# Kernel optimization log

Measured on AMD Instinct MI355X. Metric: run time of the kernel, lower is better.

The kernel has to match this reference:

```python
import jax, jax.numpy as jnp
import numpy as np

N_NODES = 100000
N_EDGES = 1600000
HID = 150
N_LAYERS = 5


def setup_inputs() -> dict:
    key = jax.random.key(0)
    ks = jax.random.split(key, 7)
    s = 1.0 / np.sqrt(HID)
    return {
        "x": jax.random.normal(ks[0], (N_NODES, HID), dtype=jnp.float32),
        "weight": jax.random.uniform(ks[1], (N_LAYERS, HID, HID), jnp.float32, -s, s),
        "w_ih": jax.random.uniform(ks[2], (3 * HID, HID), jnp.float32, -s, s),
        "w_hh": jax.random.uniform(ks[3], (3 * HID, HID), jnp.float32, -s, s),
        "b_ih": jax.random.uniform(ks[4], (3 * HID,), jnp.float32, -s, s),
        "b_hh": jax.random.uniform(ks[5], (3 * HID,), jnp.float32, -s, s),
        "edge_index": jax.random.randint(ks[6], (2, N_EDGES), 0, N_NODES, dtype=jnp.int32),
    }


def _gru_cell(inp, h, w_ih, w_hh, b_ih, b_hh):
    # torch.nn.GRUCell math
    gi = inp @ w_ih.T + b_ih            # [N, 3H]
    gh = h @ w_hh.T + b_hh              # [N, 3H]
    i_r, i_z, i_n = jnp.split(gi, 3, axis=-1)
    h_r, h_z, h_n = jnp.split(gh, 3, axis=-1)
    r = jax.nn.sigmoid(i_r + h_r)
    z = jax.nn.sigmoid(i_z + h_z)
    n = jnp.tanh(i_n + r * h_n)
    return (1.0 - z) * n + z * h


def reference(x, weight, w_ih, w_hh, b_ih, b_hh, edge_index):
    # GatedGraphConv: h'_i = GRU( sum_{j->i} (h_j @ W_l), h_i ), repeated num_layers times
    src, dst = edge_index[0], edge_index[1]
    n_nodes = x.shape[0]
    h = x
    for l in range(weight.shape[0]):
        m = h @ weight[l]                                        # [N, H] transform
        aggr = jax.ops.segment_sum(m[src], dst, num_segments=n_nodes)  # scatter-add over edges
        h = _gru_cell(aggr, h, w_ih, w_hh, b_ih, b_hh)
    return h
```

## Files before the change

kernel.cpp:

```cpp
#include <hip/hip_runtime.h>
#include <hip/hip_bf16.h>
#include <cmath>

#define HID 150
#define NN 100000
#define NE 1600000
#define NL 5
#define G3 (3*HID)
#define KP 320
#define NP 640
#define KS 10
#define BM 64
#define HSTEPS 20
#define HS_BF (20*64*8)

#define NPBSH 9
#define NBK 196
#define CAPL 64
#define CAPG 10240
#define CHUNK 4096
#define BPAD 16

typedef __hip_bfloat16 bf16;
using short8 = __attribute__((ext_vector_type(8))) short;
using f32x4  = __attribute__((ext_vector_type(4))) float;

static __device__ __forceinline__ unsigned short bf_bits(float v) {
    __hip_bfloat16 h = __float2bfloat16(v);
    return *reinterpret_cast<unsigned short*>(&h);
}

static __device__ __forceinline__ float blo(unsigned int p) {
    return __uint_as_float((p & 0xffffu) << 16);
}
static __device__ __forceinline__ float bhi(unsigned int p) {
    return __uint_as_float(p & 0xffff0000u);
}

static __device__ __forceinline__ void gld_lds16(const void* g, void* l) {
    __builtin_amdgcn_global_load_lds(
        (const __attribute__((address_space(1))) void*)g,
        (__attribute__((address_space(3))) void*)l, 16, 0, 0);
}

__global__ void build_wfrag(const float* __restrict__ W, const float* __restrict__ w_ih,
                            const float* __restrict__ w_hh, const float* __restrict__ b_ih,
                            const float* __restrict__ b_hh, bf16* __restrict__ wfrag) {
    int idx = blockIdx.x * 256 + threadIdx.x;
    if (idx >= NL * KP * NP) return;
    int j = idx % NP;
    int k = (idx / NP) % KP;
    int l = idx / (NP * KP);
    int sec = j / 160;
    int f = j - sec * 160;
    float v = 0.f;
    if (f < HID) {
        if (k < HID) {
            if (sec < 3) {
                const float* Wl = W + (size_t)l * HID * HID + (size_t)k * HID;
                const float* wr = w_ih + (size_t)(sec * HID + f) * HID;
                float acc = 0.f;
                for (int t = 0; t < HID; ++t) acc += Wl[t] * wr[t];
                v = acc;
            }
        } else if (k == HID) {
            v = (sec == 0) ? b_ih[f] + b_hh[f]
              : (sec == 1) ? b_ih[HID + f] + b_hh[HID + f]
              : (sec == 2) ? b_ih[2 * HID + f]
                           : b_hh[2 * HID + f];
        } else if (k >= 160 && k < 160 + HID) {
            int kk = k - 160;
            if (sec == 0)      v = w_hh[(size_t)f * HID + kk];
            else if (sec == 1) v = w_hh[(size_t)(HID + f) * HID + kk];
            else if (sec == 3) v = w_hh[(size_t)(2 * HID + f) * HID + kk];
        }
    }
    int kstep = k >> 5, kq = (k >> 3) & 3, ki = k & 7;
    int half = sec >> 1, s2 = sec & 1;
    int fgroup = f >> 4, nl = j & 15;
    int tl = s2 * 10 + fgroup;
    int lane = kq * 16 + nl;
    size_t addr = ((((size_t)(l * KS + kstep) * 2 + half) * 20 + tl) * 64 + lane) * 8 + ki;
    wfrag[addr] = __float2bfloat16(v);
}

__global__ __launch_bounds__(256)
void bin_edges(const int* __restrict__ ei, int* __restrict__ bcnt,
               unsigned int* __restrict__ bbuf) {
    __shared__ int lcnt[NBK];
    __shared__ unsigned int lstage[NBK * CAPL];
    int t = threadIdx.x;
    for (int i = t; i < NBK; i += 256) lcnt[i] = 0;
    __syncthreads();
    int e0 = blockIdx.x * CHUNK;
#pragma unroll
    for (int it = 0; it < CHUNK / 256; ++it) {
        int e = e0 + it * 256 + t;
        if (e < NE) {
            int src = ei[e], dst = ei[NE + e];
            int b = dst >> NPBSH;
            unsigned int v = (unsigned int)src | ((unsigned int)(dst & 511) << 17);
            int li = atomicAdd(&lcnt[b], 1);
            if (li < CAPL) {
                lstage[b * CAPL + li] = v;
            } else {
                int gp = atomicAdd(&bcnt[b * BPAD], 1);
                if (gp < CAPG) bbuf[(size_t)b * CAPG + gp] = v;
            }
        }
    }
    __syncthreads();
    int wave = t >> 6, lane = t & 63;
    for (int b = wave; b < NBK; b += 4) {
        int cnt = lcnt[b];
        if (cnt > CAPL) cnt = CAPL;
        if (cnt == 0) continue;
        int base = 0;
        if (lane == 0) base = atomicAdd(&bcnt[b * BPAD], cnt);
        base = __shfl(base, 0, 64);
        if (lane < cnt && base + lane < CAPG)
            bbuf[(size_t)b * CAPG + base + lane] = lstage[b * CAPL + lane];
    }
}

__global__ __launch_bounds__(256)
void csr_from_buckets(const int* __restrict__ bcnt, const unsigned int* __restrict__ bbuf,
                      int* __restrict__ off, int* __restrict__ csr) {
    __shared__ int hist[512];
    __shared__ int s[256];
    int b = blockIdx.x, t = threadIdx.x;
    hist[t] = 0;
    hist[256 + t] = 0;
    int base = 0;
    for (int i = 0; i < b; ++i) {
        int c = bcnt[i * BPAD];
        base += (c > CAPG) ? CAPG : c;
    }
    int cnt = bcnt[b * BPAD];
    if (cnt > CAPG) cnt = CAPG;
    __syncthreads();
    for (int i = t; i < cnt; i += 256) {
        unsigned int v = bbuf[(size_t)b * CAPG + i];
        atomicAdd(&hist[v >> 17], 1);
    }
    __syncthreads();
    int a0 = hist[2 * t], a1 = hist[2 * t + 1];
    int tsum = a0 + a1;
    s[t] = tsum;
    __syncthreads();
    for (int d = 1; d < 256; d <<= 1) {
        int u = (t >= d) ? s[t - d] : 0;
        __syncthreads();
        s[t] += u;
        __syncthreads();
    }
    int tb = base + s[t] - tsum;
    hist[2 * t] = tb;
    hist[2 * t + 1] = tb + a0;
    int node = (b << NPBSH) + 2 * t;
    if (node < NN) off[node] = tb;
    if (node + 1 < NN) off[node + 1] = tb + a0;
    if (b == NBK - 1 && t == 255) off[NN] = base + s[255];
    __syncthreads();
    for (int i = t; i < cnt; i += 256) {
        unsigned int v = bbuf[(size_t)b * CAPG + i];
        int p = atomicAdd(&hist[v >> 17], 1);
        csr[p] = (int)(v & 0x1FFFFu);
    }
}

__global__ void init_h(const float* __restrict__ x, bf16* __restrict__ Abuf) {
    size_t i = (size_t)blockIdx.x * 256 + threadIdx.x;
    if (i >= (size_t)NN * HID) return;
    int m = (int)(i / HID), f = (int)(i - (size_t)m * HID);
    Abuf[(size_t)m * KP + 160 + f] = __float2bfloat16(x[i]);
}

__global__ void aggregate(bf16* __restrict__ Abuf, const int* __restrict__ off,
                          const int* __restrict__ csr) {
    int node = (blockIdx.x * blockDim.x + threadIdx.x) >> 6;
    int lane = threadIdx.x & 63;
    if (node >= NN) return;
    int e0 = off[node], e1 = off[node + 1];
    float a0 = 0.f, a1 = 0.f, b0 = 0.f, b1 = 0.f;
    bool tail = lane < 11;
    int e = e0;
    for (; e + 4 <= e1; e += 4) {
        const unsigned int* r0 = (const unsigned int*)(Abuf + (size_t)csr[e]     * KP + 160);
        const unsigned int* r1 = (const unsigned int*)(Abuf + (size_t)csr[e + 1] * KP + 160);
        const unsigned int* r2 = (const unsigned int*)(Abuf + (size_t)csr[e + 2] * KP + 160);
        const unsigned int* r3 = (const unsigned int*)(Abuf + (size_t)csr[e + 3] * KP + 160);
        unsigned int p0 = r0[lane], p1 = r1[lane], p2 = r2[lane], p3 = r3[lane];
        unsigned int q0 = 0, q1 = 0, q2 = 0, q3 = 0;
        if (tail) { q0 = r0[64 + lane]; q1 = r1[64 + lane]; q2 = r2[64 + lane]; q3 = r3[64 + lane]; }
        a0 += blo(p0) + blo(p1) + blo(p2) + blo(p3);
        a1 += bhi(p0) + bhi(p1) + bhi(p2) + bhi(p3);
        b0 += blo(q0) + blo(q1) + blo(q2) + blo(q3);
        b1 += bhi(q0) + bhi(q1) + bhi(q2) + bhi(q3);
    }
    for (; e < e1; ++e) {
        const unsigned int* r = (const unsigned int*)(Abuf + (size_t)csr[e] * KP + 160);
        unsigned int p = r[lane];
        unsigned int q = tail ? r[64 + lane] : 0;
        a0 += blo(p); a1 += bhi(p);
        b0 += blo(q); b1 += bhi(q);
    }
    unsigned int* out = (unsigned int*)(Abuf + (size_t)node * KP);
    out[lane] = (unsigned int)bf_bits(a0) | ((unsigned int)bf_bits(a1) << 16);
    if (tail) out[64 + lane] = (unsigned int)bf_bits(b0) | ((unsigned int)bf_bits(b1) << 16);
    if (lane < 5) out[75 + lane] = (lane == 0) ? 0x00003F80u : 0u;
}

__global__ __launch_bounds__(256, 2)
void gemm_gru(const bf16* __restrict__ Abuf, const bf16* __restrict__ wfrag_l,
              float* __restrict__ h_out, bf16* __restrict__ Abuf_w, int last) {
    __shared__ __align__(16) bf16 As[KS * BM * 32];
    __shared__ __align__(16) bf16 Bs[2][HS_BF];
    int tid = threadIdx.x;
    int wave = tid >> 6, lane = tid & 63;
    int mh = wave >> 1, nh = wave & 1;
    int row0 = blockIdx.x * BM;

    {
        const char* gbase = (const char*)(Abuf + (size_t)row0 * KP);
        char* lbase = (char*)As;
#pragma unroll
        for (int it = 0; it < 10; ++it) {
            int c = it * 256 + tid;
            int ks = c >> 8;
            int rem = c & 255;
            int r = rem >> 2, qq = rem & 3;
            gld_lds16(gbase + (size_t)r * (KP * 2) + ks * 64 + qq * 16,
                      lbase + (size_t)c * 16);
        }
        const char* gb = (const char*)wfrag_l;
        char* lb = (char*)Bs[0];
#pragma unroll
        for (int it = 0; it < 5; ++it) {
            int c = it * 256 + tid;
            gld_lds16(gb + (size_t)c * 16, lb + (size_t)c * 16);
        }
    }
    __syncthreads();

    f32x4 acc[2][20];
#pragma unroll
    for (int mt = 0; mt < 2; ++mt)
#pragma unroll
        for (int t = 0; t < 20; ++t) acc[mt][t] = (f32x4){0.f, 0.f, 0.f, 0.f};

    int col = lane & 15, q = lane >> 4;
    short8 a0, a1;
    for (int hs = 0; hs < HSTEPS; ++hs) {
        int cur = hs & 1;
        if (hs < HSTEPS - 1) {
            const char* gb = (const char*)(wfrag_l + (size_t)(hs + 1) * HS_BF);
            char* lb = (char*)Bs[1 - cur];
#pragma unroll
            for (int it = 0; it < 5; ++it) {
                int c = it * 256 + tid;
                gld_lds16(gb + (size_t)c * 16, lb + (size_t)c * 16);
            }
        }
        int ks = hs >> 1, half = hs & 1;
        if (half == 0) {
            a0 = *(const short8*)(As + ((size_t)(ks * BM + mh * 32 + col) * 32 + q * 8));
            a1 = *(const short8*)(As + ((size_t)(ks * BM + mh * 32 + 16 + col) * 32 + q * 8));
        }
#pragma unroll
        for (int g = 0; g < 5; ++g) {
#pragma unroll
            for (int s2 = 0; s2 < 2; ++s2) {
                int tl = s2 * 10 + nh * 5 + g;
                short8 b = *(const short8*)(Bs[cur] + ((size_t)(tl * 64 + lane) * 8));
                int t = g * 4 + half * 2 + s2;
                acc[0][t] = __builtin_amdgcn_mfma_f32_16x16x32_bf16(a0, b, acc[0][t], 0, 0, 0);
                acc[1][t] = __builtin_amdgcn_mfma_f32_16x16x32_bf16(a1, b, acc[1][t], 0, 0, 0);
            }
        }
        __syncthreads();
    }

    int qrow = q * 4;
    bf16* Cs = &Bs[0][0];
#pragma unroll
    for (int mt = 0; mt < 2; ++mt) {
#pragma unroll
        for (int g = 0; g < 5; ++g) {
            int f = (nh * 5 + g) * 16 + col;
            if (f < HID) {
                f32x4 ar = acc[mt][g * 4 + 0], az = acc[mt][g * 4 + 1];
                f32x4 an = acc[mt][g * 4 + 2], ah = acc[mt][g * 4 + 3];
                int kh = 160 + f, ksh = kh >> 5, koff = kh & 31;
#pragma unroll
                for (int v = 0; v < 4; ++v) {
                    int rl = mh * 32 + mt * 16 + qrow + v;
                    float hp = __bfloat162float(As[((size_t)(ksh * BM) + rl) * 32 + koff]);
                    float r = 1.f / (1.f + __expf(-ar[v]));
                    float z = 1.f / (1.f + __expf(-az[v]));
                    float n = tanhf(an[v] + r * ah[v]);
                    float ho = (1.f - z) * n + z * hp;
                    if (last) {
                        int m = row0 + rl;
                        if (m < NN) h_out[(size_t)m * HID + f] = ho;
                    } else {
                        Cs[rl * 160 + f] = __float2bfloat16(ho);
                    }
                }
            }
        }
    }
    if (!last) {
        __syncthreads();
        const unsigned int* src = (const unsigned int*)Cs;
        for (int i = tid; i < 64 * 75; i += 256) {
            int r = i / 75, dw = i - r * 75;
            ((unsigned int*)(Abuf_w + (size_t)(row0 + r) * KP + 160))[dw] =
                src[r * 80 + dw];
        }
    }
}

extern "C" void kernel_launch(void* const* d_in, const int* in_sizes, int n_in,
                              void* d_out, int out_size, void* d_ws, size_t ws_size,
                              hipStream_t stream) {
    const float* x      = (const float*)d_in[0];
    const float* weight = (const float*)d_in[1];
    const float* w_ih   = (const float*)d_in[2];
    const float* w_hh   = (const float*)d_in[3];
    const float* b_ih   = (const float*)d_in[4];
    const float* b_hh   = (const float*)d_in[5];
    const int*   ei     = (const int*)d_in[6];
    float* h = (float*)d_out;

    const int nblk = (NN + BM - 1) / BM;
    const size_t NNP = (size_t)nblk * BM;
    char* p = (char*)d_ws;
    auto alloc = [&](size_t bytes) { char* r = p; p += (bytes + 255) & ~255ull; return r; };
    int*  off   = (int*)alloc((size_t)(NN + 1) * 4);
    int*  csr   = (int*)alloc((size_t)NE * 4);
    int*  bcnt  = (int*)alloc((size_t)NBK * BPAD * 4);
    unsigned int* bbuf = (unsigned int*)alloc((size_t)NBK * CAPG * 4);
    bf16* wfrag = (bf16*)alloc((size_t)NL * KS * 2 * HS_BF * 2);
    bf16* Abuf  = (bf16*)alloc((NNP + BM) * (size_t)KP * 2);

    hipMemsetAsync(bcnt, 0, (size_t)NBK * BPAD * 4, stream);
    build_wfrag<<<(NL * KP * NP + 255) / 256, 256, 0, stream>>>(weight, w_ih, w_hh, b_ih, b_hh, wfrag);
    bin_edges<<<(NE + CHUNK - 1) / CHUNK, 256, 0, stream>>>(ei, bcnt, bbuf);
    csr_from_buckets<<<NBK, 256, 0, stream>>>(bcnt, bbuf, off, csr);
    init_h<<<(int)(((size_t)NN * HID + 255) / 256), 256, 0, stream>>>(x, Abuf);

    for (int l = 0; l < NL; ++l) {
        aggregate<<<(NN * 64 + 255) / 256, 256, 0, stream>>>(Abuf, off, csr);
        gemm_gru<<<nblk, 256, 0, stream>>>(Abuf, wfrag + (size_t)l * KS * 2 * HS_BF,
                                           h, Abuf, (l == NL - 1) ? 1 : 0);
    }
}
```

Measured before the change: 1.195 ms.

## Stream A tiles through triple-buffered LDS with vmcnt-based pipelining in gemm_gru

The GEMM+GRU kernel no longer preloads the whole 64x320 A tile into LDS up front. A and B slices now go through three-stage ring buffers, prefetched two steps ahead, and explicit s_waitcnt vmcnt plus s_barrier replace __syncthreads. This shrinks LDS use, which may help occupancy, and overlaps the A loads with MFMA work. The cost is that the GRU epilogue now rereads the previous hidden state from global memory instead of LDS, and the hand-tuned vmcnt counts are fragile.

Result: faster. 1.111 ms (-7.0%).

```diff
diff --git a/kernel.cpp b/kernel.cpp
--- a/kernel.cpp
+++ b/kernel.cpp
@@ -214,34 +214,31 @@
 __global__ __launch_bounds__(256, 2)
 void gemm_gru(const bf16* __restrict__ Abuf, const bf16* __restrict__ wfrag_l,
               float* __restrict__ h_out, bf16* __restrict__ Abuf_w, int last) {
-    __shared__ __align__(16) bf16 As[KS * BM * 32];
-    __shared__ __align__(16) bf16 Bs[2][HS_BF];
+    __shared__ __align__(16) bf16 Bs[3][HS_BF];
+    __shared__ __align__(16) bf16 As3[3][BM * 32];
     int tid = threadIdx.x;
     int wave = tid >> 6, lane = tid & 63;
     int mh = wave >> 1, nh = wave & 1;
     int row0 = blockIdx.x * BM;
 
-    {
-        const char* gbase = (const char*)(Abuf + (size_t)row0 * KP);
-        char* lbase = (char*)As;
-#pragma unroll
-        for (int it = 0; it < 10; ++it) {
-            int c = it * 256 + tid;
-            int ks = c >> 8;
-            int rem = c & 255;
-            int r = rem >> 2, qq = rem & 3;
-            gld_lds16(gbase + (size_t)r * (KP * 2) + ks * 64 + qq * 16,
-                      lbase + (size_t)c * 16);
-        }
-        const char* gb = (const char*)wfrag_l;
-        char* lb = (char*)Bs[0];
+    const char* gbase = (const char*)(Abuf + (size_t)row0 * KP);
+    int ar = tid >> 2, aq = tid & 3;
+
+    auto stageB = [&](int hs) {
+        const char* gb = (const char*)(wfrag_l + (size_t)hs * HS_BF);
+        char* lb = (char*)Bs[hs % 3];
 #pragma unroll
         for (int it = 0; it < 5; ++it) {
             int c = it * 256 + tid;
             gld_lds16(gb + (size_t)c * 16, lb + (size_t)c * 16);
         }
-    }
-    __syncthreads();
+    };
+    auto stageA = [&](int ks) {
+        gld_lds16(gbase + (size_t)ar * (KP * 2) + ks * 64 + aq * 16,
+                  (char*)As3[ks % 3] + (size_t)tid * 16);
+    };
+
+    stageB(0); stageA(0); stageB(1); stageA(1);
 
     f32x4 acc[2][20];
 #pragma unroll
@@ -251,21 +248,19 @@
 
     int col = lane & 15, q = lane >> 4;
     short8 a0, a1;
+#pragma unroll
     for (int hs = 0; hs < HSTEPS; ++hs) {
-        int cur = hs & 1;
-        if (hs < HSTEPS - 1) {
-            const char* gb = (const char*)(wfrag_l + (size_t)(hs + 1) * HS_BF);
-            char* lb = (char*)Bs[1 - cur];
-#pragma unroll
-            for (int it = 0; it < 5; ++it) {
-                int c = it * 256 + tid;
-                gld_lds16(gb + (size_t)c * 16, lb + (size_t)c * 16);
-            }
-        }
-        int ks = hs >> 1, half = hs & 1;
+        if (hs < 18)       asm volatile("s_waitcnt vmcnt(6)" ::: "memory");
+        else if (hs == 18) asm volatile("s_waitcnt vmcnt(5)" ::: "memory");
+        else               asm volatile("s_waitcnt vmcnt(0)" ::: "memory");
+        __builtin_amdgcn_s_barrier();
+        __builtin_amdgcn_sched_barrier(0);
+
+        int ks = hs >> 1, half = hs & 1, cur = hs % 3;
         if (half == 0) {
-            a0 = *(const short8*)(As + ((size_t)(ks * BM + mh * 32 + col) * 32 + q * 8));
-            a1 = *(const short8*)(As + ((size_t)(ks * BM + mh * 32 + 16 + col) * 32 + q * 8));
+            const bf16* Ak = As3[ks % 3];
+            a0 = *(const short8*)(Ak + ((mh * 32 + col) * 32 + q * 8));
+            a1 = *(const short8*)(Ak + ((mh * 32 + 16 + col) * 32 + q * 8));
         }
 #pragma unroll
         for (int g = 0; g < 5; ++g) {
@@ -278,7 +273,8 @@
                 acc[1][t] = __builtin_amdgcn_mfma_f32_16x16x32_bf16(a1, b, acc[1][t], 0, 0, 0);
             }
         }
-        __syncthreads();
+        if (hs + 2 < HSTEPS) stageB(hs + 2);
+        if (half == 1 && ks + 2 < KS) stageA(ks + 2);
     }
 
     int qrow = q * 4;
@@ -289,14 +285,13 @@
         for (int g = 0; g < 5; ++g) {
             int f = (nh * 5 + g) * 16 + col;
             if (f < HID) {
-                f32x4 ar = acc[mt][g * 4 + 0], az = acc[mt][g * 4 + 1];
+                f32x4 ar4 = acc[mt][g * 4 + 0], az = acc[mt][g * 4 + 1];
                 f32x4 an = acc[mt][g * 4 + 2], ah = acc[mt][g * 4 + 3];
-                int kh = 160 + f, ksh = kh >> 5, koff = kh & 31;
 #pragma unroll
                 for (int v = 0; v < 4; ++v) {
                     int rl = mh * 32 + mt * 16 + qrow + v;
-                    float hp = __bfloat162float(As[((size_t)(ksh * BM) + rl) * 32 + koff]);
-                    float r = 1.f / (1.f + __expf(-ar[v]));
+                    float hp = __bfloat162float(Abuf[(size_t)(row0 + rl) * KP + 160 + f]);
+                    float r = 1.f / (1.f + __expf(-ar4[v]));
                     float z = 1.f / (1.f + __expf(-az[v]));
                     float n = tanhf(an[v] + r * ah[v]);
                     float ho = (1.f - z) * n + z * hp;
```
